# Kernel optimization log

Measured on AMD Instinct MI355X. Metric: run time of the kernel, lower is better.

The kernel has to match this reference:

```python
import jax, jax.numpy as jnp
import numpy as np

B, S, DM, DC, L, NS = 4, 2048, 2048, 512, 4, 5  # batch, seq, d_model, d_cortical, n_layers, n_settle


def _ln(x, g, b):
    # torch nn.LayerNorm, eps=1e-5
    m = x.mean(-1, keepdims=True)
    v = ((x - m) ** 2).mean(-1, keepdims=True)
    return (x - m) * jax.lax.rsqrt(v + 1e-5) * g + b


def setup_inputs() -> dict:
    key = jax.random.key(0)
    ks = jax.random.split(key, 20)
    f = lambda k, sh: jax.random.normal(k, sh, jnp.float32) * 0.02
    return dict(
        qwen_final_hidden=jax.random.normal(ks[0], (B, S, DM), jnp.float32),
        obs=jax.random.normal(ks[1], (4, B, S, DM), jnp.float32),
        proj_W=f(ks[2], (4, DC, DM)), proj_b=f(ks[3], (4, DC)),
        fuse_W=f(ks[4], (DC, 4 * DC)), fuse_b=f(ks[5], (DC,)),
        up_W=f(ks[6], (L, DC, DC)), up_b=f(ks[7], (L, DC)),
        lateral_W=f(ks[8], (L, DC, DC)), lateral_b=f(ks[9], (L, DC)),
        precision_logit=f(ks[10], (L, DC)),
        ln_g=jnp.ones((L, DC), jnp.float32), ln_b=jnp.zeros((L, DC), jnp.float32),
        down_W=f(ks[11], (L - 1, DC, DC)), down_b=f(ks[12], (L - 1, DC)),
        out1_W=f(ks[13], (DC, DC)), out1_b=f(ks[14], (DC,)),
        out2_W=f(ks[15], (DM, DC)), out2_b=f(ks[16], (DM,)),
    )


def reference(qwen_final_hidden, obs, proj_W, proj_b, fuse_W, fuse_b,
              up_W, up_b, lateral_W, lateral_b, precision_logit,
              ln_g, ln_b, down_W, down_b, out1_W, out1_b, out2_W, out2_b):
    b, s, dm = qwen_final_hidden.shape
    # per-observed-layer input projections, concatenated along features
    proj = jnp.einsum('obsd,ocd->bsoc', obs, proj_W) + proj_b  # (B,S,4,DC)
    cat = proj.reshape(b, s, -1)
    fused = cat @ fuse_W.T + fuse_b                             # (B,S,DC)
    x0 = fused.reshape(b * s, DC)                               # per-token cortical input

    prec = jax.nn.sigmoid(precision_logit)                      # (L,DC)

    # initial bottom-up pass: activations = compress(x)
    acts = []
    x = x0
    for i in range(L):
        x = _ln(x @ up_W[i].T + up_b[i], ln_g[i], ln_b[i])
        acts.append(x)

    # settling iterations
    for _ in range(NS):
        # top-down predictions computed from pre-sweep activations
        preds = [None] * L
        for i in range(L - 1, 0, -1):
            if i < L - 1:  # top layer has no top-down weights
                preds[i - 1] = acts[i] @ down_W[i].T + down_b[i]
        x = x0
        for i in range(L):
            compressed = _ln(x @ up_W[i].T + up_b[i], ln_g[i], ln_b[i])
            target = preds[i] if preds[i] is not None else acts[i]
            werr = (compressed - target) * prec[i]
            lateral = acts[i] @ lateral_W[i].T + lateral_b[i]
            acts[i] = _ln(acts[i] + 0.5 * werr + 0.1 * lateral, ln_g[i], ln_b[i])
            x = acts[i]

    top = acts[-1]
    h = jax.nn.gelu(top @ out1_W.T + out1_b, approximate=False)
    correction = (h @ out2_W.T + out2_b).reshape(b, s, dm)
    return qwen_final_hidden + correction
```

## Files before the change

### kernel.cpp

```cpp
#include <hip/hip_runtime.h>
#include <hip/hip_bf16.h>
#include <math.h>

#define NTOK 8192
#define DMD  2048
#define DCC  512
#define TOKH 4194304

typedef __attribute__((ext_vector_type(8))) short short8;
typedef __attribute__((ext_vector_type(4))) float f32x4;

__device__ inline float bf2f(unsigned short u) {
    union { unsigned int i; float f; } x; x.i = ((unsigned int)u) << 16; return x.f;
}
__device__ inline unsigned short f2bf(float f) {
    union { float f; unsigned int i; } x; x.f = f;
    unsigned int u = x.i;
    return (unsigned short)((u + 0x7fffu + ((u >> 16) & 1u)) >> 16);
}

typedef const __attribute__((address_space(1))) unsigned int* gas1_t;
typedef __attribute__((address_space(3))) unsigned int* las3_t;
__device__ inline void async16(const void* g, void* l) {
    __builtin_amdgcn_global_load_lds(
        (gas1_t)g,
        (las3_t)(unsigned int)(unsigned long long)l, 16, 0, 0);
}

struct CvtArgs { const float* src[7]; };

__global__ __launch_bounds__(256)
void wcvt_kernel(CvtArgs ca, unsigned short* __restrict__ dst)
{
    const int total = 2359296;
    for (int i = blockIdx.x * 256 + threadIdx.x; i < total; i += gridDim.x * 256) {
        const float* sp; int base;
        if      (i < 1048576) { sp = ca.src[0]; base = 0;       }
        else if (i < 1310720) { sp = ca.src[1]; base = 1048576; }
        else if (i < 1572864) { sp = ca.src[2]; base = 1310720; }
        else if (i < 1835008) { sp = ca.src[3]; base = 1572864; }
        else if (i < 2031616) { sp = ca.src[4]; base = 1835008; }
        else if (i < 2097152) { sp = ca.src[5]; base = 2031616; }
        else                  { sp = ca.src[6]; base = 2097152; }
        float4 v = ((const float4*)sp)[i - base];
        ushort4 o;
        o.x = f2bf(v.x); o.y = f2bf(v.y); o.z = f2bf(v.z); o.w = f2bf(v.w);
        ((ushort4*)dst)[i] = o;
    }
}

struct GArgs {
    const unsigned short* A[6];
    const unsigned short* W[6];
    const float*          bias[6];
    const float*          add[6];
    void*                 C[6];
};

template<bool A32, bool OUTF32, bool GELU>
__global__ __launch_bounds__(256)
void gemm16(GArgs ga, int lda, int ldw, int ldadd, int ldc, int K)
{
    __shared__ unsigned short As[128 * 32];
    __shared__ unsigned short Bs[128 * 32];

    const int z    = blockIdx.z;
    const int tid  = threadIdx.x;
    const int wave = tid >> 6;
    const int lane = tid & 63;
    const int bm   = blockIdx.y * 128;
    const int bn   = blockIdx.x * 128;
    const int wr   = wave >> 1;
    const int wc   = wave & 1;

    const unsigned short* Ap = ga.A[z];
    const unsigned short* Wp = ga.W[z];

    const int lrow = lane >> 2;
    const int lcol = (lane & 3) * 8;

    f32x4 acc[4][4] = {};

    for (int k0 = 0; k0 < K; k0 += 32) {
        if constexpr (A32) {
            const float* Af = (const float*)Ap;
            #pragma unroll
            for (int r = 0; r < 4; ++r) {
                int idx = r * 256 + tid;
                int row = idx >> 3, c4 = (idx & 7) * 4;
                float4 v = *(const float4*)(Af + (size_t)(bm + row) * lda + k0 + c4);
                ushort4 o;
                o.x = f2bf(v.x); o.y = f2bf(v.y); o.z = f2bf(v.z); o.w = f2bf(v.w);
                *(ushort4*)&As[row * 32 + c4] = o;
            }
        } else {
            #pragma unroll
            for (int r = 0; r < 2; ++r) {
                int c = wave + r * 4;
                async16(Ap + (size_t)(bm + c * 16 + lrow) * lda + k0 + lcol, As + c * 512);
            }
        }
        #pragma unroll
        for (int r = 0; r < 2; ++r) {
            int c = wave + r * 4;
            async16(Wp + (size_t)(bn + c * 16 + lrow) * ldw + k0 + lcol, Bs + c * 512);
        }
        __syncthreads();

        short8 af[4], bfr[4];
        #pragma unroll
        for (int i = 0; i < 4; ++i) {
            af[i]  = *(const short8*)&As[(wr * 64 + i * 16 + (lane & 15)) * 32 + (lane >> 4) * 8];
            bfr[i] = *(const short8*)&Bs[(wc * 64 + i * 16 + (lane & 15)) * 32 + (lane >> 4) * 8];
        }
        #pragma unroll
        for (int mi = 0; mi < 4; ++mi)
            #pragma unroll
            for (int ni = 0; ni < 4; ++ni)
                acc[mi][ni] = __builtin_amdgcn_mfma_f32_16x16x32_bf16(
                    af[mi], bfr[ni], acc[mi][ni], 0, 0, 0);
        __syncthreads();
    }

    const float* bias = ga.bias[z];
    const float* add  = ga.add[z];
    #pragma unroll
    for (int ni = 0; ni < 4; ++ni) {
        int col = bn + wc * 64 + ni * 16 + (lane & 15);
        float bv = bias ? bias[col] : 0.0f;
        #pragma unroll
        for (int mi = 0; mi < 4; ++mi) {
            #pragma unroll
            for (int r = 0; r < 4; ++r) {
                int row = bm + wr * 64 + mi * 16 + (lane >> 4) * 4 + r;
                float vv = acc[mi][ni][r] + bv;
                if (GELU) vv = 0.5f * vv * (1.0f + erff(vv * 0.7071067811865475f));
                if (OUTF32) {
                    if (add) vv += add[(size_t)row * ldadd + col];
                    ((float*)ga.C[z])[(size_t)row * ldc + col] = vv;
                } else {
                    ((unsigned short*)ga.C[z])[(size_t)row * ldc + col] = f2bf(vv);
                }
            }
        }
    }
}

__device__ inline int csw(int rl, int col) {
    return rl * 512 + (col ^ (((rl >> 2) & 3) << 4));
}

template<int MODE>
__global__ __launch_bounds__(256)
void gemm_fused(const unsigned short* __restrict__ Ap,
                const unsigned short* __restrict__ Wp,
                const float* __restrict__ bias,
                const float* __restrict__ g,
                const float* __restrict__ b,
                const unsigned short* a_in,
                const unsigned short* t_in,
                const unsigned short* __restrict__ lat_in,
                const float* __restrict__ logit,
                unsigned short* outp)
{
    __shared__ unsigned short As[2][32 * 32];
    __shared__ unsigned short Bs[2][512 * 32];
    __shared__ float red[2][4][32];

    const int tid  = threadIdx.x;
    const int wave = tid >> 6;
    const int lane = tid & 63;
    const int lrow = lane >> 2;
    const int lc8  = (lane & 3) * 8;
    const int bm   = blockIdx.x * 32;
    const int l15  = lane & 15;
    const int lh   = lane >> 4;

    f32x4 acc[2][8] = {};

    if (wave < 2)
        async16(Ap + (size_t)(bm + wave * 16 + lrow) * DCC + lc8, &As[0][wave * 512]);
    #pragma unroll
    for (int r = 0; r < 8; ++r)
        async16(Wp + (size_t)((r * 4 + wave) * 16 + lrow) * DCC + lc8,
                &Bs[0][(r * 4 + wave) * 512]);
    __syncthreads();

    for (int t = 0; t < 16; ++t) {
        const int cur = t & 1;
        if (t < 15) {
            const int k0 = (t + 1) * 32;
            if (wave < 2)
                async16(Ap + (size_t)(bm + wave * 16 + lrow) * DCC + k0 + lc8,
                        &As[cur ^ 1][wave * 512]);
            #pragma unroll
            for (int r = 0; r < 8; ++r)
                async16(Wp + (size_t)((r * 4 + wave) * 16 + lrow) * DCC + k0 + lc8,
                        &Bs[cur ^ 1][(r * 4 + wave) * 512]);
        }
        short8 af[2], bfr[8];
        #pragma unroll
        for (int mi = 0; mi < 2; ++mi)
            af[mi] = *(const short8*)&As[cur][(mi * 16 + l15) * 32 + lh * 8];
        #pragma unroll
        for (int ni = 0; ni < 8; ++ni)
            bfr[ni] = *(const short8*)&Bs[cur][(wave * 128 + ni * 16 + l15) * 32 + lh * 8];
        #pragma unroll
        for (int mi = 0; mi < 2; ++mi)
            #pragma unroll
            for (int ni = 0; ni < 8; ++ni)
                acc[mi][ni] = __builtin_amdgcn_mfma_f32_16x16x32_bf16(
                    af[mi], bfr[ni], acc[mi][ni], 0, 0, 0);
        __syncthreads();
    }

    float bv[8], gv[8], bbv[8];
    #pragma unroll
    for (int ni = 0; ni < 8; ++ni) {
        int col = wave * 128 + ni * 16 + l15;
        bv[ni] = bias[col]; gv[ni] = g[col]; bbv[ni] = b[col];
    }

    float ps[2][4], pq[2][4];
    #pragma unroll
    for (int mi = 0; mi < 2; ++mi)
        #pragma unroll
        for (int rr = 0; rr < 4; ++rr) {
            float s = 0.f, q = 0.f;
            #pragma unroll
            for (int ni = 0; ni < 8; ++ni) {
                float v = acc[mi][ni][rr] + bv[ni];
                acc[mi][ni][rr] = v;
                s += v; q += v * v;
            }
            #pragma unroll
            for (int off = 1; off < 16; off <<= 1) {
                s += __shfl_xor(s, off, 64);
                q += __shfl_xor(q, off, 64);
            }
            ps[mi][rr] = s; pq[mi][rr] = q;
        }
    if (l15 == 0) {
        #pragma unroll
        for (int mi = 0; mi < 2; ++mi)
            #pragma unroll
            for (int rr = 0; rr < 4; ++rr) {
                int rl = mi * 16 + lh * 4 + rr;
                red[0][wave][rl] = ps[mi][rr];
                red[1][wave][rl] = pq[mi][rr];
            }
    }
    __syncthreads();

    unsigned short* compS = &Bs[0][0];
    #pragma unroll
    for (int mi = 0; mi < 2; ++mi)
        #pragma unroll
        for (int rr = 0; rr < 4; ++rr) {
            int rl = mi * 16 + lh * 4 + rr;
            float s = red[0][0][rl] + red[0][1][rl] + red[0][2][rl] + red[0][3][rl];
            float q = red[1][0][rl] + red[1][1][rl] + red[1][2][rl] + red[1][3][rl];
            float m1 = s * (1.0f / DCC);
            float r1 = rsqrtf(q * (1.0f / DCC) - m1 * m1 + 1e-5f);
            #pragma unroll
            for (int ni = 0; ni < 8; ++ni) {
                int col = wave * 128 + ni * 16 + l15;
                compS[csw(rl, col)] = f2bf((acc[mi][ni][rr] - m1) * r1 * gv[ni] + bbv[ni]);
            }
        }
    __syncthreads();

    float gr[8], br[8], pr[8];
    if constexpr (MODE == 1) {
        const int c0 = lane * 8;
        float4 g0 = *(const float4*)(g + c0),     g1 = *(const float4*)(g + c0 + 4);
        float4 b0 = *(const float4*)(b + c0),     b1 = *(const float4*)(b + c0 + 4);
        float4 p0 = *(const float4*)(logit + c0), p1 = *(const float4*)(logit + c0 + 4);
        float gt[8] = {g0.x,g0.y,g0.z,g0.w,g1.x,g1.y,g1.z,g1.w};
        float bt[8] = {b0.x,b0.y,b0.z,b0.w,b1.x,b1.y,b1.z,b1.w};
        float pt[8] = {p0.x,p0.y,p0.z,p0.w,p1.x,p1.y,p1.z,p1.w};
        #pragma unroll
        for (int j = 0; j < 8; ++j) {
            gr[j] = gt[j]; br[j] = bt[j];
            pr[j] = 1.0f / (1.0f + __expf(-pt[j]));
        }
    }

    #pragma unroll
    for (int rr = 0; rr < 8; ++rr) {
        const int rl = wave * 8 + rr;
        const size_t gbase = (size_t)(bm + rl) * DCC + lane * 8;
        short8 cm = *(const short8*)&compS[csw(rl, lane * 8)];
        if constexpr (MODE == 0) {
            *(short8*)(outp + gbase) = cm;
        } else {
            short8 ar = *(const short8*)(a_in + gbase);
            short8 tr = *(const short8*)(t_in + gbase);
            short8 lr = *(const short8*)(lat_in + gbase);
            float tv[8], s = 0.f, q = 0.f;
            #pragma unroll
            for (int j = 0; j < 8; ++j) {
                float val = bf2f((unsigned short)ar[j])
                          + 0.5f * (bf2f((unsigned short)cm[j]) - bf2f((unsigned short)tr[j])) * pr[j]
                          + 0.1f * bf2f((unsigned short)lr[j]);
                tv[j] = val; s += val; q += val * val;
            }
            #pragma unroll
            for (int off = 1; off < 64; off <<= 1) {
                s += __shfl_xor(s, off, 64);
                q += __shfl_xor(q, off, 64);
            }
            float m2 = s * (1.0f / DCC);
            float r2 = rsqrtf(q * (1.0f / DCC) - m2 * m2 + 1e-5f);
            short8 o;
            #pragma unroll
            for (int j = 0; j < 8; ++j)
                o[j] = (short)f2bf((tv[j] - m2) * r2 * gr[j] + br[j]);
            *(short8*)(outp + gbase) = o;
        }
    }
}

extern "C" void kernel_launch(void* const* d_in, const int* in_sizes, int n_in,
                              void* d_out, int out_size, void* d_ws, size_t ws_size,
                              hipStream_t stream)
{
    const float* qwen   = (const float*)d_in[0];
    const float* obs    = (const float*)d_in[1];
    const float* proj_W = (const float*)d_in[2];
    const float* proj_b = (const float*)d_in[3];
    const float* fuse_W = (const float*)d_in[4];
    const float* fuse_b = (const float*)d_in[5];
    const float* up_W   = (const float*)d_in[6];
    const float* up_b   = (const float*)d_in[7];
    const float* lat_W  = (const float*)d_in[8];
    const float* lat_b  = (const float*)d_in[9];
    const float* plogit = (const float*)d_in[10];
    const float* ln_g   = (const float*)d_in[11];
    const float* ln_b   = (const float*)d_in[12];
    const float* down_W = (const float*)d_in[13];
    const float* down_b = (const float*)d_in[14];
    const float* out1_W = (const float*)d_in[15];
    const float* out1_b = (const float*)d_in[16];
    const float* out2_W = (const float*)d_in[17];
    const float* out2_b = (const float*)d_in[18];
    float* out = (float*)d_out;

    unsigned short* wsu = (unsigned short*)d_ws;
    unsigned short* catbuf = wsu;
    unsigned short* x0b    = wsu + 16777216;
    unsigned short* acts16[4] = {
        wsu + 20971520, wsu + 20971520 + TOKH,
        wsu + 20971520 + 2 * TOKH, wsu + 20971520 + 3 * TOKH };
    unsigned short* w16    = wsu + 37748736;
    unsigned short* projW16 = w16;
    unsigned short* fuseW16 = w16 + 4194304;
    unsigned short* upW16   = w16 + 5242880;
    unsigned short* latW16  = w16 + 6291456;
    unsigned short* downW16 = w16 + 7340032;
    unsigned short* out1W16 = w16 + 8126464;
    unsigned short* out2W16 = w16 + 8388608;
    unsigned short* h16     = catbuf;

    unsigned short* outu = (unsigned short*)d_out;
    unsigned short* pred16a = outu;
    unsigned short* pred16b = outu + TOKH;
    unsigned short* lat16[4] = { outu + 2*TOKH, outu + 3*TOKH, outu + 4*TOKH, outu + 5*TOKH };

    dim3 blk(256);

    {
        CvtArgs ca;
        ca.src[0] = proj_W; ca.src[1] = fuse_W; ca.src[2] = up_W;
        ca.src[3] = lat_W;  ca.src[4] = down_W; ca.src[5] = out1_W;
        ca.src[6] = out2_W;
        wcvt_kernel<<<dim3(2048), blk, 0, stream>>>(ca, w16);
    }

    {
        GArgs a{};
        for (int o = 0; o < 4; ++o) {
            a.A[o]    = (const unsigned short*)(obs + (size_t)o * NTOK * DMD);
            a.W[o]    = projW16 + (size_t)o * DCC * DMD;
            a.bias[o] = proj_b + o * DCC;
            a.C[o]    = catbuf + o * DCC;
        }
        gemm16<true, false, false><<<dim3(DCC/128, NTOK/128, 4), blk, 0, stream>>>(
            a, DMD, DMD, 0, 4 * DCC, DMD);
    }
    {
        GArgs a{};
        a.A[0] = catbuf; a.W[0] = fuseW16; a.bias[0] = fuse_b; a.C[0] = x0b;
        gemm16<false, false, false><<<dim3(DCC/128, NTOK/128, 1), blk, 0, stream>>>(
            a, 4 * DCC, 4 * DCC, 0, DCC, 4 * DCC);
    }

    for (int i = 0; i < 4; ++i) {
        gemm_fused<0><<<dim3(NTOK/32), blk, 0, stream>>>(
            (i == 0) ? x0b : acts16[i - 1],
            upW16 + (size_t)i * DCC * DCC, up_b + i * DCC,
            ln_g + i * DCC, ln_b + i * DCC,
            nullptr, nullptr, nullptr, nullptr, acts16[i]);
    }

    for (int s = 0; s < 5; ++s) {
        {
            GArgs a{};
            a.A[0] = acts16[1]; a.W[0] = downW16 + (size_t)1 * DCC * DCC;
            a.bias[0] = down_b + 1 * DCC; a.C[0] = pred16a;
            a.A[1] = acts16[2]; a.W[1] = downW16 + (size_t)2 * DCC * DCC;
            a.bias[1] = down_b + 2 * DCC; a.C[1] = pred16b;
            for (int i = 0; i < 4; ++i) {
                a.A[2 + i] = acts16[i];
                a.W[2 + i] = latW16 + (size_t)i * DCC * DCC;
                a.bias[2 + i] = lat_b + i * DCC;
                a.C[2 + i] = lat16[i];
            }
            gemm16<false, false, false><<<dim3(DCC/128, NTOK/128, 6), blk, 0, stream>>>(
                a, DCC, DCC, 0, DCC, DCC);
        }
        for (int i = 0; i < 4; ++i) {
            const unsigned short* tgt =
                (i == 0) ? pred16a : (i == 1) ? pred16b : acts16[i];
            gemm_fused<1><<<dim3(NTOK/32), blk, 0, stream>>>(
                (i == 0) ? x0b : acts16[i - 1],
                upW16 + (size_t)i * DCC * DCC, up_b + i * DCC,
                ln_g + i * DCC, ln_b + i * DCC,
                acts16[i], tgt, lat16[i], plogit + i * DCC, acts16[i]);
        }
    }

    {
        GArgs a{};
        a.A[0] = acts16[3]; a.W[0] = out1W16; a.bias[0] = out1_b; a.C[0] = h16;
        gemm16<false, false, true><<<dim3(DCC/128, NTOK/128, 1), blk, 0, stream>>>(
            a, DCC, DCC, 0, DCC, DCC);
    }
    {
        GArgs a{};
        a.A[0] = h16; a.W[0] = out2W16; a.bias[0] = out2_b;
        a.add[0] = qwen; a.C[0] = out;
        gemm16<false, true, false><<<dim3(DMD/128, NTOK/128, 1), blk, 0, stream>>>(
            a, DCC, DCC, DMD, DMD, DCC);
    }
}
```

Measured before the change: 1.683 ms.

## Pre-convert obs to bf16 in two halves and swizzle GEMM block order

Replaces the in-GEMM fp32-to-bf16 conversion of the obs operand with a separate conversion kernel that writes bf16 into the output buffer as scratch, done in two halves of two observed layers each. The projection GEMM then uses async global-to-LDS loads for A as well. A block-index swizzle is added to all GEMMs to improve L2 reuse. This removes the per-tile redundant conversion of A, which was re-read once per N-block, at the cost of an extra full read and write of obs.

```diff
diff --git a/kernel.cpp b/kernel.cpp
--- a/kernel.cpp
+++ b/kernel.cpp
@@ -25,6 +25,17 @@
     __builtin_amdgcn_global_load_lds(
         (gas1_t)g,
         (las3_t)(unsigned int)(unsigned long long)l, 16, 0, 0);
+}
+
+__global__ __launch_bounds__(256)
+void cvt_kernel(const float* __restrict__ s, unsigned short* __restrict__ d, int n4)
+{
+    int i = blockIdx.x * 256 + threadIdx.x;
+    if (i >= n4) return;
+    float4 v = ((const float4*)s)[i];
+    ushort4 o;
+    o.x = f2bf(v.x); o.y = f2bf(v.y); o.z = f2bf(v.z); o.w = f2bf(v.w);
+    ((ushort4*)d)[i] = o;
 }
 
 struct CvtArgs { const float* src[7]; };
@@ -57,7 +68,7 @@
     void*                 C[6];
 };
 
-template<bool A32, bool OUTF32, bool GELU>
+template<bool OUTF32, bool GELU>
 __global__ __launch_bounds__(256)
 void gemm16(GArgs ga, int lda, int ldw, int ldadd, int ldc, int K)
 {
@@ -68,8 +79,13 @@
     const int tid  = threadIdx.x;
     const int wave = tid >> 6;
     const int lane = tid & 63;
-    const int bm   = blockIdx.y * 128;
-    const int bn   = blockIdx.x * 128;
+
+    const int nwg   = gridDim.x * gridDim.y;
+    const int bid   = blockIdx.y * gridDim.x + blockIdx.x;
+    const int swz   = (bid & 7) * (nwg >> 3) + (bid >> 3);
+    const int bn    = (swz % gridDim.x) * 128;
+    const int bm    = (swz / gridDim.x) * 128;
+
     const int wr   = wave >> 1;
     const int wc   = wave & 1;
 
@@ -82,27 +98,10 @@
     f32x4 acc[4][4] = {};
 
     for (int k0 = 0; k0 < K; k0 += 32) {
-        if constexpr (A32) {
-            const float* Af = (const float*)Ap;
-            #pragma unroll
-            for (int r = 0; r < 4; ++r) {
-                int idx = r * 256 + tid;
-                int row = idx >> 3, c4 = (idx & 7) * 4;
-                float4 v = *(const float4*)(Af + (size_t)(bm + row) * lda + k0 + c4);
-                ushort4 o;
-                o.x = f2bf(v.x); o.y = f2bf(v.y); o.z = f2bf(v.z); o.w = f2bf(v.w);
-                *(ushort4*)&As[row * 32 + c4] = o;
-            }
-        } else {
-            #pragma unroll
-            for (int r = 0; r < 2; ++r) {
-                int c = wave + r * 4;
-                async16(Ap + (size_t)(bm + c * 16 + lrow) * lda + k0 + lcol, As + c * 512);
-            }
-        }
         #pragma unroll
         for (int r = 0; r < 2; ++r) {
             int c = wave + r * 4;
+            async16(Ap + (size_t)(bm + c * 16 + lrow) * lda + k0 + lcol, As + c * 512);
             async16(Wp + (size_t)(bn + c * 16 + lrow) * ldw + k0 + lcol, Bs + c * 512);
         }
         __syncthreads();
@@ -377,21 +376,25 @@
         wcvt_kernel<<<dim3(2048), blk, 0, stream>>>(ca, w16);
     }
 
-    {
+    for (int p = 0; p < 2; ++p) {
+        int n4 = (2 * NTOK * DMD) / 4;
+        cvt_kernel<<<dim3((n4 + 255) / 256), blk, 0, stream>>>(
+            obs + (size_t)p * 2 * NTOK * DMD, outu, n4);
         GArgs a{};
-        for (int o = 0; o < 4; ++o) {
-            a.A[o]    = (const unsigned short*)(obs + (size_t)o * NTOK * DMD);
-            a.W[o]    = projW16 + (size_t)o * DCC * DMD;
-            a.bias[o] = proj_b + o * DCC;
-            a.C[o]    = catbuf + o * DCC;
-        }
-        gemm16<true, false, false><<<dim3(DCC/128, NTOK/128, 4), blk, 0, stream>>>(
+        for (int q = 0; q < 2; ++q) {
+            int o = 2 * p + q;
+            a.A[q]    = outu + (size_t)q * NTOK * DMD;
+            a.W[q]    = projW16 + (size_t)o * DCC * DMD;
+            a.bias[q] = proj_b + o * DCC;
+            a.C[q]    = catbuf + o * DCC;
+        }
+        gemm16<false, false><<<dim3(DCC/128, NTOK/128, 2), blk, 0, stream>>>(
             a, DMD, DMD, 0, 4 * DCC, DMD);
     }
     {
         GArgs a{};
         a.A[0] = catbuf; a.W[0] = fuseW16; a.bias[0] = fuse_b; a.C[0] = x0b;
-        gemm16<false, false, false><<<dim3(DCC/128, NTOK/128, 1), blk, 0, stream>>>(
+        gemm16<false, false><<<dim3(DCC/128, NTOK/128, 1), blk, 0, stream>>>(
             a, 4 * DCC, 4 * DCC, 0, DCC, 4 * DCC);
     }
 
@@ -416,7 +419,7 @@
                 a.bias[2 + i] = lat_b + i * DCC;
                 a.C[2 + i] = lat16[i];
             }
-            gemm16<false, false, false><<<dim3(DCC/128, NTOK/128, 6), blk, 0, stream>>>(
+            gemm16<false, false><<<dim3(DCC/128, NTOK/128, 6), blk, 0, stream>>>(
                 a, DCC, DCC, 0, DCC, DCC);
         }
         for (int i = 0; i < 4; ++i) {
@@ -433,14 +436,14 @@
     {
         GArgs a{};
         a.A[0] = acts16[3]; a.W[0] = out1W16; a.bias[0] = out1_b; a.C[0] = h16;
-        gemm16<false, false, true><<<dim3(DCC/128, NTOK/128, 1), blk, 0, stream>>>(
+        gemm16<false, true><<<dim3(DCC/128, NTOK/128, 1), blk, 0, stream>>>(
             a, DCC, DCC, 0, DCC, DCC);
     }
     {
         GArgs a{};
         a.A[0] = h16; a.W[0] = out2W16; a.bias[0] = out2_b;
         a.add[0] = qwen; a.C[0] = out;
-        gemm16<false, true, false><<<dim3(DMD/128, NTOK/128, 1), blk, 0, stream>>>(
+        gemm16<true, false><<<dim3(DMD/128, NTOK/128, 1), blk, 0, stream>>>(
             a, DCC, DCC, DMD, DMD, DCC);
     }
 }
```

Result: faster. 1.595 ms (-5.2%).
